# Kernel tuning notes

Measured on AMD Instinct MI355X. Metric: run time of the kernel, lower is better.

## Reference

```python
import jax, jax.numpy as jnp
import numpy as np
import math

MU = 0.1
NU = 10.0
UNITS = [512] * 8
FEATURES = 1024
BATCH = 8192
EPS = 1e-5


def _norm(x):
    return jnp.linalg.norm(x) + EPS


def _cayley(W):
    # Cayley orthogonalization; matches the torch reference (recursive transpose for wide matrices).
    cout, cin = W.shape
    if cin > cout:
        return _cayley(W.T).T
    U, V = W[:cin], W[cin:]
    I = jnp.eye(cin, dtype=W.dtype)
    A = U - U.T + V.T @ V
    iIpA = jnp.linalg.inv(I + A)
    return jnp.concatenate([iIpA @ (I - A), -2.0 * V @ iIpA], axis=0)


def setup_inputs() -> dict:
    key = jax.random.key(0)
    ks = jax.random.split(key, 5)
    sum_units = sum(UNITS)
    # xavier-normal-ish scales
    x = jax.random.normal(ks[0], (BATCH, FEATURES), jnp.float32)
    Fq = jax.random.normal(ks[1], (sum_units, FEATURES), jnp.float32) * math.sqrt(2.0 / (sum_units + FEATURES))
    fq = _norm(Fq).reshape(1)  # init.constant_(fq, norm(Fq))
    by = jnp.zeros((FEATURES,), jnp.float32)
    nz = UNITS[0]
    Fr0 = jax.random.normal(ks[2], (nz, nz), jnp.float32) * math.sqrt(2.0 / (nz + nz))
    Fr_rest = jax.random.normal(ks[3], (len(UNITS) - 1, nz, 2 * nz), jnp.float32) * math.sqrt(2.0 / (nz + 2 * nz))
    fr0 = _norm(Fr0).reshape(1)
    fr_rest = jnp.linalg.norm(Fr_rest, axis=(1, 2)) + EPS
    fr = jnp.concatenate([fr0, fr_rest])
    b = jnp.zeros((len(UNITS), nz), jnp.float32)
    return {"x": x, "Fq": Fq, "fq": fq, "by": by, "Fr0": Fr0, "Fr_rest": Fr_rest, "fr": fr, "b": b}


def reference(x, Fq, fq, by, Fr0, Fr_rest, fr, b):
    sqrt_gam = math.sqrt(NU - MU)
    sqrt2 = math.sqrt(2.0)
    # per-forward Cayley orthogonalization (training path)
    Q = _cayley(fq[0] * Fq / _norm(Fq))  # (sum_units, features)
    Rs = [_cayley(fr[0] * Fr0 / _norm(Fr0))]
    for k in range(Fr_rest.shape[0]):
        Rs.append(_cayley(fr[k + 1] * Fr_rest[k] / _norm(Fr_rest[k])))

    xh = sqrt_gam * (x @ Q.T)  # (B, sum_units)
    yh = []
    hk_1 = xh[..., :0]  # empty start
    idx = 0
    for k, nz in enumerate(UNITS):
        xk = xh[..., idx:idx + nz]
        pre = sqrt2 * (jnp.concatenate([xk, hk_1], axis=-1) @ Rs[k].T) + b[k]
        gh = sqrt2 * (jax.nn.relu(pre) @ Rs[k])  # (B, nz + nz_prev)
        hk = gh[..., :nz] - xk
        gk = gh[..., nz:]
        yh.append(hk_1 - gk)
        idx += nz
        hk_1 = hk
    yh.append(hk_1)
    yh = jnp.concatenate(yh, axis=-1)  # (B, sum_units)
    return 0.5 * ((MU + NU) * x + sqrt_gam * (yh @ Q)) + by
```

## Files before the change

### kernel.cpp

```cpp
#include <hip/hip_runtime.h>
#include <math.h>


using s8v = __attribute__((ext_vector_type(8))) short;
using f4v = __attribute__((ext_vector_type(4))) float;
typedef unsigned short ush;
typedef unsigned int uint32;

#define DEV __device__ __forceinline__

DEV float b2f(ush u){ union{unsigned int i; float f;} v; v.i = ((unsigned int)u)<<16; return v.f; }
DEV ush f2b(float f){
  union{float f; unsigned int i;} v; v.f = f;
  unsigned int u = v.i;
  return (ush)((u + 0x7fffu + ((u>>16)&1u)) >> 16);
}

typedef __attribute__((address_space(1))) void gvoid;
typedef __attribute__((address_space(3))) void lvoid;
DEV void gload16(const void* g, void* l){
  __builtin_amdgcn_global_load_lds((gvoid*)g, (lvoid*)l, 16, 0, 0);
}

DEV void st16(ush* dst, const ush* a){
  *(int4*)dst = *(const int4*)a; *(int4*)(dst+8) = *(const int4*)(a+8);
}

struct GA {
  const ush *A0h, *A0l; long lda0;
  const ush *A1h, *A1l; long lda1; int ksplit;
  const ush *Bh, *Bl; long ldb;
  int K, M, N;
  float alpha, beta;
  long sA, sB, sO, sD;
  void *o0,*o1,*o2,*o3,*o4;
  const void *e0,*e1;
  long ldo0, ldo1, ldE;
};

enum { E_F32=0, E_BF16=1, E_BF16T2=2, E_SPLIT=3, E_QW=4, E_PRE=5, E_GH=6, E_OUT=7 };

template<int BM, int BN, int EPI, bool SPLIT, bool TRX>
__global__ __launch_bounds__(256) void gemm_k(GA gq, GA gr, int zsplit)
{
  constexpr int AH = BM*32;
  constexpr int BH = BN*32;
  constexpr int PANEL = (AH+BH) * (SPLIT ? 2 : 1);
  constexpr int DEPTH = (PANEL <= 6144) ? 2 : 1;
  constexpr int NBUF  = DEPTH + 2;
  constexpr int TBN = TRX ? 64*65*2 : 0;
  constexpr int SMN = (NBUF*PANEL > TBN) ? NBUF*PANEL : TBN;
  __shared__ ush smem[SMN] __attribute__((aligned(16)));
  uint32* tb = (uint32*)smem;

  constexpr int LPS = (BM/64 + BN/64) * (SPLIT ? 2 : 1);

  GA g; int bz;
  if ((int)blockIdx.z < zsplit){ g = gq; bz = blockIdx.z; }
  else                         { g = gr; bz = blockIdx.z - zsplit; }

  const int gx = gridDim.x, gy = gridDim.y;
  const int lin = blockIdx.y*gx + blockIdx.x;
  const int per = gx*8;
  const int grp = lin / per;
  const int rem = lin - grp*per;
  int gh = gy - grp*8; if (gh > 8) gh = 8;
  const int by = grp*8 + rem % gh;
  const int bx = rem / gh;
  const int m0 = by * BM;
  const int n0 = bx * BN;
  if (m0 >= g.M || n0 >= g.N) return;

  const int t = threadIdx.x;
  const int lane = t & 63;
  const int wave = t >> 6;
  const int wm = (wave >> 1) * (BM/2);
  const int wn = (wave & 1) * (BN/2);
  constexpr int MT = BM/32;
  constexpr int NT = BN/32;

  const ush* Ah  = g.A0h + (long)bz*g.sA;
  const ush* Alp = SPLIT ? g.A0l + (long)bz*g.sA : nullptr;
  const ush* Bhp = g.Bh  + (long)bz*g.sB;
  const ush* Blp = SPLIT ? g.Bl  + (long)bz*g.sB : nullptr;

  f4v acc[MT][NT];
  #pragma unroll
  for (int i=0;i<MT;i++)
    #pragma unroll
    for (int j=0;j<NT;j++) acc[i][j] = f4v{0.f,0.f,0.f,0.f};

  const int sr  = lane >> 2;
  const int scg = lane & 3;

  auto STAGE = [&](int k0, int nb){
    ush* dA  = smem + nb*PANEL;
    ush* dB  = dA + AH;
    ush* dAl = dB + BH;
    ush* dBl = dAl + AH;
    #pragma unroll
    for (int p = 0; p < BM/64; ++p) {
      const int lr = wave*16 + sr + p*64;
      const int gc = scg ^ ((lr>>1)&3);
      const int kc = k0 + gc*8;
      long aoff; const ush* gp;
      if (kc < g.ksplit){ aoff = (long)(m0+lr)*g.lda0 + kc;               gp = Ah + aoff; }
      else              { aoff = (long)(m0+lr)*g.lda1 + (kc - g.ksplit);  gp = g.A1h + aoff; }
      gload16(gp, &dA[(wave*16 + p*64)*32]);
      if (SPLIT) gload16(Alp + aoff, &dAl[(wave*16 + p*64)*32]);
    }
    #pragma unroll
    for (int p = 0; p < BN/64; ++p) {
      const int lr = wave*16 + sr + p*64;
      const int gc = scg ^ ((lr>>1)&3);
      const long boff = (long)(n0+lr)*g.ldb + k0 + gc*8;
      gload16(Bhp + boff, &dB[(wave*16 + p*64)*32]);
      if (SPLIT) gload16(Blp + boff, &dBl[(wave*16 + p*64)*32]);
    }
  };

  STAGE(0, 0);
  if (DEPTH == 2 && g.K > 32) STAGE(32, 1);
  int cur = 0;
  for (int k0 = 0; k0 < g.K; k0 += 32) {
    const int rem_steps = ((g.K - k0) >> 5) - 1;
    if (DEPTH == 2) {
      if (rem_steps >= 2) {
        const int nb = (cur+2 >= NBUF) ? cur+2-NBUF : cur+2;
        STAGE(k0 + 64, nb);
        asm volatile("s_waitcnt vmcnt(%0)" :: "n"(2*LPS) : "memory");
      } else if (rem_steps == 1) {
        asm volatile("s_waitcnt vmcnt(%0)" :: "n"(LPS) : "memory");
      } else {
        asm volatile("s_waitcnt vmcnt(0)" ::: "memory");
      }
    } else {
      if (rem_steps >= 1) {
        const int nb = (cur+1 >= NBUF) ? cur+1-NBUF : cur+1;
        STAGE(k0 + 32, nb);
        asm volatile("s_waitcnt vmcnt(%0)" :: "n"(LPS) : "memory");
      } else {
        asm volatile("s_waitcnt vmcnt(0)" ::: "memory");
      }
    }
    __builtin_amdgcn_sched_barrier(0);
    __builtin_amdgcn_s_barrier();
    __builtin_amdgcn_sched_barrier(0);

    const ush* rA  = smem + cur*PANEL;
    const ush* rB  = rA + AH;
    const ush* rAl = rB + BH;
    const ush* rBl = rAl + AH;

    const int fr = lane & 15;
    const int cc = lane >> 4;
    s8v af[MT], bf_[NT];
    #pragma unroll
    for (int i=0;i<MT;i++){ const int row = wm + i*16 + fr;
      af[i] = *(const s8v*)(&rA[row*32 + ((cc ^ ((row>>1)&3))<<3)]); }
    #pragma unroll
    for (int j=0;j<NT;j++){ const int row = wn + j*16 + fr;
      bf_[j] = *(const s8v*)(&rB[row*32 + ((cc ^ ((row>>1)&3))<<3)]); }
    #pragma unroll
    for (int i=0;i<MT;i++)
      #pragma unroll
      for (int j=0;j<NT;j++)
        acc[i][j] = __builtin_amdgcn_mfma_f32_16x16x32_bf16(af[i], bf_[j], acc[i][j], 0,0,0);
    if (SPLIT) {
      s8v al2[MT], bl2[NT];
      #pragma unroll
      for (int j=0;j<NT;j++){ const int row = wn + j*16 + fr;
        bl2[j] = *(const s8v*)(&rBl[row*32 + ((cc ^ ((row>>1)&3))<<3)]); }
      #pragma unroll
      for (int i=0;i<MT;i++){ const int row = wm + i*16 + fr;
        al2[i] = *(const s8v*)(&rAl[row*32 + ((cc ^ ((row>>1)&3))<<3)]); }
      #pragma unroll
      for (int i=0;i<MT;i++)
        #pragma unroll
        for (int j=0;j<NT;j++)
          acc[i][j] = __builtin_amdgcn_mfma_f32_16x16x32_bf16(af[i], bl2[j], acc[i][j], 0,0,0);
      #pragma unroll
      for (int i=0;i<MT;i++)
        #pragma unroll
        for (int j=0;j<NT;j++)
          acc[i][j] = __builtin_amdgcn_mfma_f32_16x16x32_bf16(al2[i], bf_[j], acc[i][j], 0,0,0);
    }
    cur = (cur+1 >= NBUF) ? 0 : cur+1;
  }

  if constexpr (TRX) __syncthreads();

  #pragma unroll
  for (int i=0;i<MT;i++)
    #pragma unroll
    for (int j=0;j<NT;j++)
      #pragma unroll
      for (int r=0;r<4;r++) {
        const int lrow = wm + i*16 + ((lane>>4)<<2) + r;
        const int lcol = wn + j*16 + (lane & 15);
        const int grow = m0 + lrow;
        const int gcol = n0 + lcol;
        float v = g.alpha * acc[i][j][r];
        if constexpr (EPI == E_F32) {
          if (g.e0) v += g.beta * ((const float*)g.e0)[(long)bz*g.sD + (long)grow*g.ldo0 + gcol];
          ((float*)g.o0)[(long)bz*g.sO + (long)grow*g.ldo0 + gcol] = v;
        } else if constexpr (EPI == E_BF16) {
          if (g.e0) v += g.beta * b2f(((const ush*)g.e0)[(long)bz*g.sD + (long)grow*g.ldo0 + gcol]);
          ((ush*)g.o0)[(long)bz*g.sO + (long)grow*g.ldo0 + gcol] = f2b(v);
        } else if constexpr (EPI == E_BF16T2) {
          if (g.e0) v += g.beta * b2f(((const ush*)g.e0)[(long)bz*g.sD + (long)grow*g.ldo0 + gcol]);
          ush hv = f2b(v);
          ((ush*)g.o0)[(long)bz*g.sO + (long)grow*g.ldo0 + gcol] = hv;
          tb[lrow*65 + lcol] = hv;
        } else if constexpr (EPI == E_SPLIT) {
          if (g.e0) v += g.beta * ((const float*)g.e0)[(long)bz*g.sD + (long)grow*g.ldo0 + gcol];
          if (g.o0) ((float*)g.o0)[(long)bz*g.sO + (long)grow*g.ldo0 + gcol] = v;
          ush hv = f2b(v);
          ush lv = f2b(v - b2f(hv));
          ((ush*)g.o1)[(long)bz*g.sO + (long)grow*g.ldo0 + gcol] = hv;
          ((ush*)g.o2)[(long)bz*g.sO + (long)grow*g.ldo0 + gcol] = lv;
          if (TRX) tb[lrow*65 + lcol] = (uint32)hv | ((uint32)lv<<16);
        } else if constexpr (EPI == E_QW) {
          ush hv = f2b(v);
          ((ush*)g.o0)[(long)bz*g.sO + (long)grow*g.ldo0 + gcol] = hv;
          tb[lrow*65 + lcol] = hv;
        } else if constexpr (EPI == E_PRE) {
          v += ((const float*)g.e0)[gcol];
          v = v > 0.f ? v : 0.f;
          ((ush*)g.o0)[(long)grow*g.ldo0 + gcol] = f2b(v);
        } else if constexpr (EPI == E_GH) {
          if (gcol < 512) {
            float h = v - b2f(((const ush*)g.e0)[(long)grow*g.ldE + gcol]);
            ush hb = f2b(h);
            ((ush*)g.o0)[(long)grow*512 + gcol] = hb;
            if (g.o2) ((ush*)g.o2)[(long)grow*4096 + gcol] = hb;
          } else {
            float y = b2f(((const ush*)g.e1)[(long)grow*512 + (gcol-512)]) - v;
            ((ush*)g.o1)[(long)grow*4096 + (gcol-512)] = f2b(y);
          }
        } else if constexpr (EPI == E_OUT) {
          float o = 0.5f*(10.1f*((const float*)g.e0)[(long)grow*1024 + gcol] + v)
                  + ((const float*)g.e1)[gcol];
          ((float*)g.o0)[(long)grow*1024 + gcol] = o;
        }
      }

  if constexpr (TRX) {
    __syncthreads();
    const int tr  = t >> 2;
    const int seg = t & 3;
    uint32 vals[16];
    #pragma unroll
    for (int u=0;u<16;u++) vals[u] = tb[(seg*16+u)*65 + tr];
    ush hb[16] __attribute__((aligned(16)));
    ush lb[16] __attribute__((aligned(16)));
    #pragma unroll
    for (int u=0;u<16;u++){ hb[u] = (ush)(vals[u]&0xffffu); lb[u] = (ush)(vals[u]>>16); }
    const long bT = (long)bz*g.sO + (long)(n0+tr)*g.ldo1 + m0 + seg*16;
    if constexpr (EPI == E_BF16T2) {
      st16((ush*)g.o1 + bT, hb);
    } else if constexpr (EPI == E_SPLIT) {
      if (g.o3) { st16((ush*)g.o3 + bT, hb); st16((ush*)g.o4 + bT, lb); }
    } else if constexpr (EPI == E_QW) {
      st16((ush*)g.o1 + bT, hb);
    }
  }
}


__global__ __launch_bounds__(256) void k_norms(const float* __restrict__ Fq,
    const float* __restrict__ Fr0, const float* __restrict__ Frr, float* s2){
  const int y = blockIdx.y;
  const float* p; long cnt4;
  if (y==0){ p=Fq; cnt4=1048576l; }
  else if (y==1){ p=Fr0; cnt4=65536l; }
  else { p=Frr + (long)(y-2)*524288; cnt4=131072l; }
  float s = 0.f;
  for (long i = (long)blockIdx.x*256 + threadIdx.x; i < cnt4; i += (long)gridDim.x*256){
    float4 v = ((const float4*)p)[i];
    s += v.x*v.x + v.y*v.y + v.z*v.z + v.w*v.w;
  }
  #pragma unroll
  for (int o=32;o>0;o>>=1) s += __shfl_down(s, o, 64);
  __shared__ float red[4];
  if ((threadIdx.x & 63)==0) red[threadIdx.x>>6] = s;
  __syncthreads();
  if (threadIdx.x==0) atomicAdd(&s2[y], red[0]+red[1]+red[2]+red[3]);
}

__global__ void k_scales(const float* s2, const float* fq, const float* fr, float* sc){
  int t = threadIdx.x;
  if (t < 9){
    float v = (t==0)? fq[0] : fr[t-1];
    sc[t] = v / (sqrtf(s2[t]) + 1e-5f);
  }
}

__global__ __launch_bounds__(256) void k_buildT(const float* __restrict__ Fq,
    const float* __restrict__ Frr, const float* sc,
    ush* Vh, ush* Vl, ush* Vth, ush* Vtl,
    ush* Wrh, ush* Wrl, ush* WrTh, ush* WrTl){
  __shared__ uint32 tb[64*65];
  const int z = blockIdx.z;
  const int r = threadIdx.x >> 2;
  const int cs = (threadIdx.x & 3)*16;
  ush hh[16] __attribute__((aligned(16)));
  ush ll[16] __attribute__((aligned(16)));
  if (z==0){
    const long r0 = (long)blockIdx.y*64, c0 = (long)blockIdx.x*64;
    const float s = sc[0];
    const float* src = &Fq[(1024+r0+r)*1024 + c0 + cs];
    #pragma unroll
    for (int u=0;u<16;u++){
      float v = s*src[u];
      ush h = f2b(v); ush l = f2b(v - b2f(h));
      hh[u]=h; ll[u]=l;
      tb[r*65 + cs + u] = (uint32)h | ((uint32)l<<16);
    }
    st16(&Vh[(r0+r)*1024 + c0 + cs], hh);
    st16(&Vl[(r0+r)*1024 + c0 + cs], ll);
    __syncthreads();
    const int tr = threadIdx.x>>2, seg = threadIdx.x&3;
    #pragma unroll
    for (int u=0;u<16;u++){
      uint32 v = tb[(seg*16+u)*65 + tr];
      hh[u]=(ush)(v&0xffffu); ll[u]=(ush)(v>>16);
    }
    st16(&Vth[(c0+tr)*3072 + r0 + seg*16], hh);
    st16(&Vtl[(c0+tr)*3072 + r0 + seg*16], ll);
  } else {
    if (blockIdx.x>=8 || blockIdx.y>=8) return;
    const int k = z-1;
    const long r0 = (long)blockIdx.y*64, c0 = (long)blockIdx.x*64;
    const float s = sc[2+k];
    const float* src = &Frr[(long)k*524288 + (r0+r)*1024 + 512 + c0 + cs];
    #pragma unroll
    for (int u=0;u<16;u++){
      float v = s*src[u];
      ush h = f2b(v); ush l = f2b(v - b2f(h));
      hh[u]=h; ll[u]=l;
      tb[r*65 + cs + u] = (uint32)h | ((uint32)l<<16);
    }
    st16(&Wrh[(long)k*262144 + (r0+r)*512 + c0 + cs], hh);
    st16(&Wrl[(long)k*262144 + (r0+r)*512 + c0 + cs], ll);
    __syncthreads();
    const int tr = threadIdx.x>>2, seg = threadIdx.x&3;
    #pragma unroll
    for (int u=0;u<16;u++){
      uint32 v = tb[(seg*16+u)*65 + tr];
      hh[u]=(ush)(v&0xffffu); ll[u]=(ush)(v>>16);
    }
    st16(&WrTh[(long)k*262144 + (c0+tr)*512 + r0 + seg*16], hh);
    st16(&WrTl[(long)k*262144 + (c0+tr)*512 + r0 + seg*16], ll);
  }
}

__global__ __launch_bounds__(256) void k_asmT(const float* __restrict__ Fq,
    const float* __restrict__ Fr0, const float* __restrict__ Frr,
    const float* sc, const float* __restrict__ PP,
    ush* Mh, ush* Ml, ush* MTh, ush* MTl){
  __shared__ uint32 tb[64*65];
  const int z = blockIdx.z;
  const int r = threadIdx.x >> 2;
  const int cs = (threadIdx.x & 3)*16;
  const long ROFF = 1048576l, RS = 262144l;
  long r0 = (long)blockIdx.y*64, c0 = (long)blockIdx.x*64;
  const float* dsrc; const float* msrc; const float* psrc = nullptr;
  float s; long obase; long old_; float sgn;
  if (z==0){
    s = sc[0]; sgn = 1.f;
    dsrc = &Fq[(r0+r)*1024 + c0 + cs];
    msrc = &Fq[(c0+r)*1024 + r0 + cs];
    psrc = &PP[(r0+r)*1024 + c0 + cs];
    obase = 0; old_ = 1024;
  } else {
    if (blockIdx.x>=8 || blockIdx.y>=8) return;
    const int b = z-1;
    if (b==0){
      s = sc[1]; sgn = 1.f;
      dsrc = &Fr0[(r0+r)*512 + c0 + cs];
      msrc = &Fr0[(c0+r)*512 + r0 + cs];
    } else {
      s = sc[1+b]; sgn = -1.f;
      const float* W = Frr + (long)(b-1)*524288;
      dsrc = &W[(r0+r)*1024 + c0 + cs];
      msrc = &W[(c0+r)*1024 + r0 + cs];
      psrc = &PP[ROFF + (long)(b-1)*RS + (r0+r)*512 + c0 + cs];
    }
    obase = ROFF + (long)b*RS; old_ = 512;
  }
  #pragma unroll
  for (int u=0;u<16;u++) tb[r*65 + cs + u] = __float_as_uint(msrc[u]);
  __syncthreads();
  ush hh[16] __attribute__((aligned(16)));
  ush ll[16] __attribute__((aligned(16)));
  #pragma unroll
  for (int u=0;u<16;u++){
    const int c = cs + u;
    float mir = __uint_as_float(tb[c*65 + r]);
    float a = sgn * s * (dsrc[u] - mir);
    if (psrc) a += psrc[u];
    float m = ((r0 + r == c0 + c) ? 1.f : 0.f) + a;
    ush h = f2b(m); ush l = f2b(m - b2f(h));
    hh[u]=h; ll[u]=l;
  }
  st16(&Mh[obase + (r0+r)*old_ + c0 + cs], hh);
  st16(&Ml[obase + (r0+r)*old_ + c0 + cs], ll);
  __syncthreads();
  #pragma unroll
  for (int u=0;u<16;u++) tb[r*65 + cs + u] = (uint32)hh[u] | ((uint32)ll[u]<<16);
  __syncthreads();
  const int tr = threadIdx.x>>2, seg = threadIdx.x&3;
  #pragma unroll
  for (int u=0;u<16;u++){
    uint32 v = tb[(seg*16+u)*65 + tr];
    hh[u]=(ush)(v&0xffffu); ll[u]=(ush)(v>>16);
  }
  st16(&MTh[obase + (c0+tr)*old_ + r0 + seg*16], hh);
  st16(&MTl[obase + (c0+tr)*old_ + r0 + seg*16], ll);
}

__global__ __launch_bounds__(256) void k_rowabs(const float* __restrict__ T2, float* bmax){
  const int y = blockIdx.y;
  const float* row; int n;
  if (y==0){ row = T2 + (long)blockIdx.x*1024; n = 1024; }
  else { if (blockIdx.x >= 512) return;
         row = T2 + 1048576l + (long)(y-1)*262144 + (long)blockIdx.x*512; n = 512; }
  float s=0.f;
  for (int i=threadIdx.x;i<n;i+=256) s += fabsf(row[i]);
  #pragma unroll
  for (int o=32;o>0;o>>=1) s += __shfl_down(s,o,64);
  __shared__ float red[4];
  if ((threadIdx.x&63)==0) red[threadIdx.x>>6]=s;
  __syncthreads();
  if (threadIdx.x==0){
    float tot = red[0]+red[1]+red[2]+red[3];
    atomicMax((unsigned int*)&bmax[y], __float_as_uint(tot));
  }
}

__global__ void k_makec(const float* bmax, float* cvl){
  int t=threadIdx.x;
  if (t<9){
    float bnd = sqrtf(fmaxf(bmax[t], 1.f));
    cvl[t] = 1.9f/(1.f + bnd);
  }
}

__global__ __launch_bounds__(256) void k_initX(const ush* __restrict__ Mh,
    const ush* __restrict__ MTh, const float* cvl, ush* Xh, ush* XTh){
  long i = (long)blockIdx.x*256 + threadIdx.x;
  int b = (i < 1048576l) ? 0 : 1 + (int)((i - 1048576l) >> 18);
  float c = cvl[b];
  Xh[i]  = f2b(c * b2f(MTh[i]));
  XTh[i] = f2b(c * b2f(Mh[i]));
}

__global__ __launch_bounds__(256) void k_promote(const ush* __restrict__ Xh,
    float* Xf, ush* Xl, ush* XTl){
  long i = (long)blockIdx.x*256 + threadIdx.x;
  Xf[i] = b2f(Xh[i]);
  Xl[i] = 0; XTl[i] = 0;
}

__global__ __launch_bounds__(256) void k_topT(const ush* __restrict__ Xh, const ush* __restrict__ Xl,
    ush* Qb, ush* QTb, ush* RK, ush* RKT){
  __shared__ uint32 tb[64*65];
  const int z = blockIdx.z;
  const int r = threadIdx.x >> 2;
  const int cs = (threadIdx.x & 3)*16;
  const long ROFF = 1048576l, RS = 262144l;
  long r0 = (long)blockIdx.y*64, c0 = (long)blockIdx.x*64;
  ush hh[16] __attribute__((aligned(16)));
  if (z==0){
    const long base = (r0+r)*1024 + c0 + cs;
    #pragma unroll
    for (int u=0;u<16;u++){
      float v = 2.f*(b2f(Xh[base+u]) + b2f(Xl[base+u])) - ((r0+r == c0+cs+u)?1.f:0.f);
      hh[u] = f2b(v);
      tb[r*65 + cs + u] = hh[u];
    }
    st16(&Qb[(r0+r)*1024 + c0 + cs], hh);
    __syncthreads();
    const int tr = threadIdx.x>>2, seg = threadIdx.x&3;
    #pragma unroll
    for (int u=0;u<16;u++) hh[u] = (ush)tb[(seg*16+u)*65 + tr];
    st16(&QTb[(c0+tr)*4096 + r0 + seg*16], hh);
  } else {
    if (blockIdx.x>=8 || blockIdx.y>=8) return;
    const int b = z-1;
    const long base = ROFF + (long)b*RS + (r0+r)*512 + c0 + cs;
    #pragma unroll
    for (int u=0;u<16;u++){
      float v = 2.f*(b2f(Xh[base+u]) + b2f(Xl[base+u])) - ((r0+r == c0+cs+u)?1.f:0.f);
      hh[u] = f2b(v);
      tb[r*65 + cs + u] = hh[u];
    }
    st16(&RKT[(long)b*524288 + (r0+r)*512 + c0 + cs], hh);
    __syncthreads();
    const int tr = threadIdx.x>>2, seg = threadIdx.x&3;
    #pragma unroll
    for (int u=0;u<16;u++) hh[u] = (ush)tb[(seg*16+u)*65 + tr];
    st16(&RK[(long)b*524288 + (c0+tr)*1024 + r0 + seg*16], hh);
  }
}

__global__ __launch_bounds__(256) void k_f2bf(const float* __restrict__ in, ush* __restrict__ o){
  long i = ((long)blockIdx.x*256 + threadIdx.x)*8;
  float4 a = *(const float4*)(in+i);
  float4 b = *(const float4*)(in+i+4);
  ush u[8] __attribute__((aligned(16)));
  u[0]=f2b(a.x);u[1]=f2b(a.y);u[2]=f2b(a.z);u[3]=f2b(a.w);
  u[4]=f2b(b.x);u[5]=f2b(b.y);u[6]=f2b(b.z);u[7]=f2b(b.w);
  *(int4*)(o+i) = *(const int4*)u;
}


static GA mk(const ush* Ah, const ush* Al, long lda,
             const ush* Bh, const ush* Bl, long ldb,
             int K, int M, int N, float alpha){
  GA g{}; g.ksplit=1<<30; g.A0h=Ah; g.A0l=Al; g.lda0=lda;
  g.Bh=Bh; g.Bl=Bl; g.ldb=ldb; g.K=K; g.M=M; g.N=N; g.alpha=alpha; g.beta=0.f;
  return g;
}

extern "C" void kernel_launch(void* const* d_in, const int* in_sizes, int n_in,
                              void* d_out, int out_size, void* d_ws, size_t ws_size,
                              hipStream_t stream)
{
  (void)in_sizes; (void)n_in; (void)out_size; (void)ws_size;
  const float* x   = (const float*)d_in[0];
  const float* Fq  = (const float*)d_in[1];
  const float* fqp = (const float*)d_in[2];
  const float* by  = (const float*)d_in[3];
  const float* Fr0 = (const float*)d_in[4];
  const float* Frr = (const float*)d_in[5];
  const float* frp = (const float*)d_in[6];
  const float* bp  = (const float*)d_in[7];
  float* out = (float*)d_out;

  const float SQG = sqrtf(10.0f - 0.1f);
  const float SQ2 = sqrtf(2.0f);
  const long UN = 3145728l;
  const long ROFF = 1048576l, RS = 262144l;

  char* base = (char*)d_ws;
  size_t off = 0;
  auto alloc = [&](size_t bytes)->char*{
    char* p = base + off; off = (off + bytes + 255) & ~(size_t)255; return p;
  };

  ush* Qb  = (ush*)alloc(4194304l*2);
  ush* QTb = (ush*)alloc(4194304l*2);
  ush* RK  = (ush*)alloc(4194304l*2);
  ush* RKT = (ush*)alloc(4194304l*2);
  ush* xbf = (ush*)alloc(8388608l*2);
  float* scal = (float*)alloc(256*4);
  float* s2   = scal;
  float* bmax = scal + 16;
  float* cvl  = scal + 32;
  float* sc   = scal + 48;

  const size_t scratch0 = off;
  ush* Vh   = (ush*)alloc(UN*2);
  ush* Vl   = (ush*)alloc(UN*2);
  ush* Vth  = (ush*)alloc(UN*2);
  ush* Vtl  = (ush*)alloc(UN*2);
  ush* Wrh  = (ush*)alloc(1835008l*2);
  ush* Wrl  = (ush*)alloc(1835008l*2);
  ush* WrTh = (ush*)alloc(1835008l*2);
  ush* WrTl = (ush*)alloc(1835008l*2);
  float* PPf = (float*)alloc(UN*4);
  ush* Mh  = (ush*)alloc(UN*2);
  ush* Ml  = (ush*)alloc(UN*2);
  ush* MTh = (ush*)alloc(UN*2);
  ush* MTl = (ush*)alloc(UN*2);
  ush* Sh  = (ush*)alloc(UN*2);
  ush* XhA = (ush*)alloc(UN*2);
  ush* XhB = (ush*)alloc(UN*2);
  ush* XlA = (ush*)alloc(UN*2);
  ush* XlB = (ush*)alloc(UN*2);
  ush* XThA = (ush*)alloc(UN*2);
  ush* XThB = (ush*)alloc(UN*2);
  ush* XTlA = (ush*)alloc(UN*2);
  ush* XTlB = (ush*)alloc(UN*2);
  float* XfA = (float*)alloc(UN*4);
  float* XfB = (float*)alloc(UN*4);
  ush* Yh  = (ush*)alloc(UN*2);
  ush* Yl  = (ush*)alloc(UN*2);

  ush* Xh[2]  = {XhA, XhB};
  ush* Xl[2]  = {XlA, XlB};
  ush* XTh[2] = {XThA, XThB};
  ush* XTl[2] = {XTlA, XTlB};
  float* Xf[2] = {XfA, XfB};

  dim3 B256(256);
  GA ga{}, gr{};

  (void)hipMemsetAsync(scal, 0, 1024, stream);
  k_norms<<<dim3(256,9),B256,0,stream>>>(Fq, Fr0, Frr, s2);
  k_scales<<<1,16,0,stream>>>(s2, fqp, frp, sc);

  k_buildT<<<dim3(16,48,8),B256,0,stream>>>(Fq, Frr, sc, Vh,Vl,Vth,Vtl, Wrh,Wrl,WrTh,WrTl);

  ga = mk(Vth,Vtl,3072, Vth,Vtl,3072, 3072,1024,1024, 1.f); ga.o0=PPf; ga.ldo0=1024;
  gr = mk(Wrh,Wrl,512, Wrh,Wrl,512, 512,512,512, 1.f);
  gr.sA=RS; gr.sB=RS; gr.o0=PPf+ROFF; gr.sO=RS; gr.ldo0=512;
  gemm_k<64,64,E_F32,true,false><<<dim3(16,16,8),B256,0,stream>>>(ga,gr,1);

  k_asmT<<<dim3(16,16,9),B256,0,stream>>>(Fq, Fr0, Frr, sc, PPf, Mh,Ml,MTh,MTl);

  ga = mk(Mh,nullptr,1024, Mh,nullptr,1024, 1024,1024,1024, 1.f); ga.o0=Sh; ga.ldo0=1024;
  gr = mk(Mh+ROFF,nullptr,512, Mh+ROFF,nullptr,512, 512,512,512, 1.f);
  gr.sA=RS; gr.sB=RS; gr.o0=Sh+ROFF; gr.sO=RS; gr.ldo0=512;
  gemm_k<64,64,E_BF16,false,false><<<dim3(16,16,9),B256,0,stream>>>(ga,gr,1);

  ga = mk(Sh,nullptr,1024, Sh,nullptr,1024, 1024,1024,1024, 1.f); ga.o0=PPf; ga.ldo0=1024;
  gr = mk(Sh+ROFF,nullptr,512, Sh+ROFF,nullptr,512, 512,512,512, 1.f);
  gr.sA=RS; gr.sB=RS; gr.o0=PPf+ROFF; gr.sO=RS; gr.ldo0=512;
  gemm_k<64,64,E_F32,false,false><<<dim3(16,16,9),B256,0,stream>>>(ga,gr,1);
  k_rowabs<<<dim3(1024,9),B256,0,stream>>>(PPf, bmax);
  k_makec<<<1,16,0,stream>>>(bmax, cvl);
  k_initX<<<12288,B256,0,stream>>>(Mh, MTh, cvl, Xh[0], XTh[0]);

  int cur = 0;
  for (int it=0; it<9; ++it){
    int nxt = cur^1;
    ga = mk(XTh[cur],nullptr,1024, Mh,nullptr,1024, 1024,1024,1024, 1.f); ga.o0=Yh; ga.ldo0=1024;
    gr = mk(XTh[cur]+ROFF,nullptr,512, Mh+ROFF,nullptr,512, 512,512,512, 1.f);
    gr.sA=RS; gr.sB=RS; gr.o0=Yh+ROFF; gr.sO=RS; gr.ldo0=512;
    gemm_k<64,64,E_BF16,false,false><<<dim3(16,16,9),B256,0,stream>>>(ga,gr,1);

    ga = mk(Xh[cur],nullptr,1024, Yh,nullptr,1024, 1024,1024,1024, -1.f);
    ga.beta=2.f; ga.e0=Xh[cur];
    ga.o0=Xh[nxt]; ga.o1=XTh[nxt]; ga.ldo0=1024; ga.ldo1=1024;
    gr = mk(Xh[cur]+ROFF,nullptr,512, Yh+ROFF,nullptr,512, 512,512,512, -1.f);
    gr.beta=2.f; gr.e0=Xh[cur]+ROFF; gr.sD=RS;
    gr.sA=RS; gr.sB=RS; gr.sO=RS;
    gr.o0=Xh[nxt]+ROFF; gr.o1=XTh[nxt]+ROFF; gr.ldo0=512; gr.ldo1=512;
    gemm_k<64,64,E_BF16T2,false,true><<<dim3(16,16,9),B256,0,stream>>>(ga,gr,1);
    cur = nxt;
  }

  k_promote<<<12288,B256,0,stream>>>(Xh[cur], Xf[cur], Xl[cur], XTl[cur]);
  for (int it=0; it<2; ++it){
    int nxt = cur^1;
    ga = mk(XTh[cur],XTl[cur],1024, Mh,Ml,1024, 1024,1024,1024, 1.f);
    ga.o1=Yh; ga.o2=Yl; ga.ldo0=1024;
    gr = mk(XTh[cur]+ROFF,XTl[cur]+ROFF,512, Mh+ROFF,Ml+ROFF,512, 512,512,512, 1.f);
    gr.sA=RS; gr.sB=RS; gr.o1=Yh+ROFF; gr.o2=Yl+ROFF; gr.sO=RS; gr.ldo0=512;
    gemm_k<64,64,E_SPLIT,true,false><<<dim3(16,16,9),B256,0,stream>>>(ga,gr,1);

    ga = mk(Xh[cur],Xl[cur],1024, Yh,Yl,1024, 1024,1024,1024, -1.f);
    ga.beta=2.f; ga.e0=Xf[cur];
    ga.o0=Xf[nxt]; ga.o1=Xh[nxt]; ga.o2=Xl[nxt]; ga.o3=XTh[nxt]; ga.o4=XTl[nxt];
    ga.ldo0=1024; ga.ldo1=1024;
    gr = mk(Xh[cur]+ROFF,Xl[cur]+ROFF,512, Yh+ROFF,Yl+ROFF,512, 512,512,512, -1.f);
    gr.beta=2.f; gr.e0=Xf[cur]+ROFF; gr.sD=RS;
    gr.sA=RS; gr.sB=RS; gr.sO=RS;
    gr.o0=Xf[nxt]+ROFF; gr.o1=Xh[nxt]+ROFF; gr.o2=Xl[nxt]+ROFF;
    gr.o3=XTh[nxt]+ROFF; gr.o4=XTl[nxt]+ROFF;
    gr.ldo0=512; gr.ldo1=512;
    gemm_k<64,64,E_SPLIT,true,true><<<dim3(16,16,9),B256,0,stream>>>(ga,gr,1);
    cur = nxt;
  }

  k_topT<<<dim3(16,16,9),B256,0,stream>>>(Xh[cur], Xl[cur], Qb, QTb, RK, RKT);

  ga = mk(Vh,Vl,1024, XTh[cur],XTl[cur],1024, 1024,3072,1024, -2.f);
  ga.o0=Qb + 1048576l; ga.ldo0=1024; ga.o1=QTb + 1024; ga.ldo1=4096;
  gr = mk(WrTh,WrTl,512, XTh[cur]+ROFF+RS, XTl[cur]+ROFF+RS, 512, 512,512,512, -2.f);
  gr.sA=RS; gr.sB=RS; gr.sO=524288;
  gr.o0=RKT + 524288 + 262144; gr.ldo0=512;
  gr.o1=RK + 524288 + 512; gr.ldo1=1024;
  gemm_k<64,64,E_QW,true,true><<<dim3(16,48,8),B256,0,stream>>>(ga,gr,1);

  off = scratch0;
  ush* xh  = (ush*)alloc(33554432l*2);
  ush* yh  = (ush*)alloc(33554432l*2);
  ush* pre = (ush*)alloc(4194304l*2);
  ush* h0  = (ush*)alloc(4194304l*2);
  ush* h1  = (ush*)alloc(4194304l*2);

  k_f2bf<<<4096,B256,0,stream>>>(x, xbf);
  ga = mk(xbf,nullptr,1024, Qb,nullptr,1024, 1024,8192,4096, SQG);
  ga.o0=xh; ga.ldo0=4096;
  gemm_k<128,128,E_BF16,false,false><<<dim3(32,64,1),B256,0,stream>>>(ga,ga,1);

  for (int k=0;k<8;++k){
    ush* hprev = (k==0)? nullptr : (((k-1)&1) ? h1 : h0);
    ush* hnew  = (k&1) ? h1 : h0;
    GA gp_ = mk(xh + (long)k*512, nullptr, 4096,
                (k==0)? RKT : RK + (long)k*524288, nullptr, (k==0)?512:1024,
                (k==0)?512:1024, 8192, 512, SQ2);
    gp_.ksplit = 512; gp_.A1h = hprev; gp_.lda1 = 512;
    gp_.e0 = bp + (long)k*512; gp_.o0 = pre; gp_.ldo0 = 512;
    gemm_k<128,64,E_PRE,false,false><<<dim3(8,64,1),B256,0,stream>>>(gp_,gp_,1);

    GA gg = mk(pre, nullptr, 512,
               (k==0)? RK : RKT + (long)k*524288, nullptr, (k==0)?1024:512,
               512, 8192, (k==0)?512:1024, SQ2);
    gg.e0 = xh + (long)k*512; gg.ldE = 4096;
    gg.e1 = hprev;
    gg.o0 = hnew;
    gg.o1 = (k>=1)? (void*)(yh + (long)(k-1)*512) : nullptr;
    gg.o2 = (k==7)? (void*)(yh + 3584) : nullptr;
    if (k==0) gemm_k<128,64,E_GH,false,false><<<dim3(8,64,1),B256,0,stream>>>(gg,gg,1);
    else      gemm_k<128,128,E_GH,false,false><<<dim3(8,64,1),B256,0,stream>>>(gg,gg,1);
  }

  ga = mk(yh,nullptr,4096, QTb,nullptr,4096, 4096,8192,1024, SQG);
  ga.e0=x; ga.e1=by; ga.o0=out; ga.ldo0=1024;
  gemm_k<128,128,E_OUT,false,false><<<dim3(8,64,1),B256,0,stream>>>(ga,ga,1);
}
```

Before: 1.464 ms.

## Fuse Newton-Schulz iterations into one persistent kernel with grid barriers

Replaces the 18 separate GEMM launches of the nine bf16 Newton-Schulz iterations with a single persistent kernel of 768 blocks. The blocks sync through a hierarchical atomic grid barrier in global memory (32-block groups, then a global counter). This removes per-launch overhead and tail effects. It relies on all 768 blocks being co-resident, otherwise it deadlocks. It also lowers the shared-memory double-buffer threshold in the generic GEMM template.

New measurement: 3.192 ms. 2.18x slower.

```diff
diff --git a/kernel.cpp b/kernel.cpp
--- a/kernel.cpp
+++ b/kernel.cpp
@@ -46,7 +46,7 @@
   constexpr int AH = BM*32;
   constexpr int BH = BN*32;
   constexpr int PANEL = (AH+BH) * (SPLIT ? 2 : 1);
-  constexpr int DEPTH = (PANEL <= 6144) ? 2 : 1;
+  constexpr int DEPTH = (PANEL <= 4096) ? 2 : 1;
   constexpr int NBUF  = DEPTH + 2;
   constexpr int TBN = TRX ? 64*65*2 : 0;
   constexpr int SMN = (NBUF*PANEL > TBN) ? NBUF*PANEL : TBN;
@@ -267,6 +267,147 @@
   }
 }
 
+__global__ __launch_bounds__(256) void ns_fused(
+    const ush* __restrict__ Mh, ush* XhA, ush* XThA, ush* XhB, ush* XThB,
+    ush* Yh, uint32* bar, int iters)
+{
+  constexpr int PANEL = 4096;
+  constexpr int NBUF  = 4;
+  __shared__ ush smem[NBUF*PANEL] __attribute__((aligned(16)));
+  uint32* tb = (uint32*)smem;
+
+  const int b = blockIdx.x;
+  const int tri = b/3, rph = b - tri*3;
+  int m0, n0, ld, K; long base;
+  if (rph == 0){
+    m0 = (tri>>4)<<6; n0 = (tri&15)<<6; base = 0; ld = 1024; K = 1024;
+  } else {
+    const int rj = tri*2 + rph - 1;
+    const int z = rj>>6, idx = rj&63;
+    m0 = (idx>>3)<<6; n0 = (idx&7)<<6;
+    base = 1048576l + (long)z*262144l; ld = 512; K = 512;
+  }
+
+  const int t = threadIdx.x, lane = t&63, wave = t>>6;
+  const int wm = (wave>>1)*32, wn = (wave&1)*32;
+  const int sr = lane>>2, scg = lane&3;
+  const int fr = lane&15, cc = lane>>4;
+
+  int barno = 0;
+  auto gbar = [&](){
+    __syncthreads();
+    if (t == 0){
+      const int grp = b >> 5;
+      uint32 v = __hip_atomic_fetch_add(&bar[64 + grp*32], 1u,
+                    __ATOMIC_RELEASE, __HIP_MEMORY_SCOPE_AGENT);
+      if (v == 31u){
+        __hip_atomic_store(&bar[64 + grp*32], 0u,
+                    __ATOMIC_RELAXED, __HIP_MEMORY_SCOPE_AGENT);
+        uint32 r = __hip_atomic_fetch_add(&bar[16], 1u,
+                    __ATOMIC_ACQ_REL, __HIP_MEMORY_SCOPE_AGENT);
+        if (r == 23u){
+          __hip_atomic_store(&bar[16], 0u,
+                    __ATOMIC_RELAXED, __HIP_MEMORY_SCOPE_AGENT);
+          __hip_atomic_fetch_add(&bar[32], 1u,
+                    __ATOMIC_RELEASE, __HIP_MEMORY_SCOPE_AGENT);
+        }
+      }
+      while ((int)__hip_atomic_load(&bar[32],
+                    __ATOMIC_ACQUIRE, __HIP_MEMORY_SCOPE_AGENT) <= barno)
+        __builtin_amdgcn_s_sleep(2);
+      __threadfence();
+    }
+    __syncthreads();
+    ++barno;
+  };
+
+  auto run_gemm = [&](const ush* A, const ush* B, bool g2,
+                      const ush* e0, ush* o0, ush* oT){
+    f4v acc[2][2];
+    #pragma unroll
+    for (int i=0;i<2;i++)
+      #pragma unroll
+      for (int j=0;j<2;j++) acc[i][j] = f4v{0.f,0.f,0.f,0.f};
+    auto STAGE = [&](int k0, int nb){
+      ush* dA = smem + nb*PANEL;
+      ush* dB = dA + 2048;
+      const int lr = wave*16 + sr;
+      const int gc = scg ^ ((lr>>1)&3);
+      gload16(A + (long)(m0+lr)*ld + k0 + gc*8, &dA[lr*32]);
+      gload16(B + (long)(n0+lr)*ld + k0 + gc*8, &dB[lr*32]);
+    };
+    STAGE(0,0); STAGE(32,1);
+    int cur = 0;
+    for (int k0 = 0; k0 < K; k0 += 32){
+      const int rem = ((K - k0) >> 5) - 1;
+      if (rem >= 2){ STAGE(k0+64, (cur+2)&3);
+        asm volatile("s_waitcnt vmcnt(4)" ::: "memory"); }
+      else if (rem == 1){ asm volatile("s_waitcnt vmcnt(2)" ::: "memory"); }
+      else { asm volatile("s_waitcnt vmcnt(0)" ::: "memory"); }
+      __builtin_amdgcn_sched_barrier(0);
+      __builtin_amdgcn_s_barrier();
+      __builtin_amdgcn_sched_barrier(0);
+      const ush* rA = smem + cur*PANEL;
+      const ush* rB = rA + 2048;
+      s8v af[2], bf_[2];
+      #pragma unroll
+      for (int i=0;i<2;i++){ const int row = wm+i*16+fr;
+        af[i] = *(const s8v*)&rA[row*32 + ((cc ^ ((row>>1)&3))<<3)]; }
+      #pragma unroll
+      for (int j=0;j<2;j++){ const int row = wn+j*16+fr;
+        bf_[j] = *(const s8v*)&rB[row*32 + ((cc ^ ((row>>1)&3))<<3)]; }
+      #pragma unroll
+      for (int i=0;i<2;i++)
+        #pragma unroll
+        for (int j=0;j<2;j++)
+          acc[i][j] = __builtin_amdgcn_mfma_f32_16x16x32_bf16(af[i],bf_[j],acc[i][j],0,0,0);
+      cur = (cur+1)&3;
+    }
+    if (g2) __syncthreads();
+    #pragma unroll
+    for (int i=0;i<2;i++)
+      #pragma unroll
+      for (int j=0;j<2;j++)
+        #pragma unroll
+        for (int r=0;r<4;r++){
+          const int lrow = wm + i*16 + ((lane>>4)<<2) + r;
+          const int lcol = wn + j*16 + fr;
+          const long off = (long)(m0+lrow)*ld + n0 + lcol;
+          if (!g2){
+            o0[off] = f2b(acc[i][j][r]);
+          } else {
+            float v = 2.f*b2f(e0[off]) - acc[i][j][r];
+            ush hv = f2b(v);
+            o0[off] = hv;
+            tb[lrow*65 + lcol] = hv;
+          }
+        }
+    if (g2){
+      __syncthreads();
+      const int tr = t>>2, seg = t&3;
+      uint32 vals[16];
+      #pragma unroll
+      for (int u=0;u<16;u++) vals[u] = tb[(seg*16+u)*65 + tr];
+      ush hb[16] __attribute__((aligned(16)));
+      #pragma unroll
+      for (int u=0;u<16;u++) hb[u] = (ush)vals[u];
+      st16(oT + (long)(n0+tr)*ld + m0 + seg*16, hb);
+    }
+  };
+
+  ush* X[2]  = {XhA, XhB};
+  ush* XT[2] = {XThA, XThB};
+  int cur = 0;
+  for (int it = 0; it < iters; ++it){
+    run_gemm(XT[cur] + base, Mh + base, false, nullptr, Yh + base, nullptr);
+    gbar();
+    run_gemm(X[cur] + base, Yh + base, true, X[cur] + base,
+             X[cur^1] + base, XT[cur^1] + base);
+    if (it != iters-1) gbar();
+    cur ^= 1;
+  }
+}
+
 
 __global__ __launch_bounds__(256) void k_norms(const float* __restrict__ Fq,
     const float* __restrict__ Fr0, const float* __restrict__ Frr, float* s2){
@@ -560,6 +701,7 @@
   float* bmax = scal + 16;
   float* cvl  = scal + 32;
   float* sc   = scal + 48;
+  uint32* bar = (uint32*)alloc(4096);
 
   const size_t scratch0 = off;
   ush* Vh   = (ush*)alloc(UN*2);
@@ -599,6 +741,7 @@
   GA ga{}, gr{};
 
   (void)hipMemsetAsync(scal, 0, 1024, stream);
+  (void)hipMemsetAsync(bar, 0, 4096, stream);
   k_norms<<<dim3(256,9),B256,0,stream>>>(Fq, Fr0, Frr, s2);
   k_scales<<<1,16,0,stream>>>(s2, fqp, frp, sc);
 
@@ -624,24 +767,8 @@
   k_makec<<<1,16,0,stream>>>(bmax, cvl);
   k_initX<<<12288,B256,0,stream>>>(Mh, MTh, cvl, Xh[0], XTh[0]);
 
-  int cur = 0;
-  for (int it=0; it<9; ++it){
-    int nxt = cur^1;
-    ga = mk(XTh[cur],nullptr,1024, Mh,nullptr,1024, 1024,1024,1024, 1.f); ga.o0=Yh; ga.ldo0=1024;
-    gr = mk(XTh[cur]+ROFF,nullptr,512, Mh+ROFF,nullptr,512, 512,512,512, 1.f);
-    gr.sA=RS; gr.sB=RS; gr.o0=Yh+ROFF; gr.sO=RS; gr.ldo0=512;
-    gemm_k<64,64,E_BF16,false,false><<<dim3(16,16,9),B256,0,stream>>>(ga,gr,1);
-
-    ga = mk(Xh[cur],nullptr,1024, Yh,nullptr,1024, 1024,1024,1024, -1.f);
-    ga.beta=2.f; ga.e0=Xh[cur];
-    ga.o0=Xh[nxt]; ga.o1=XTh[nxt]; ga.ldo0=1024; ga.ldo1=1024;
-    gr = mk(Xh[cur]+ROFF,nullptr,512, Yh+ROFF,nullptr,512, 512,512,512, -1.f);
-    gr.beta=2.f; gr.e0=Xh[cur]+ROFF; gr.sD=RS;
-    gr.sA=RS; gr.sB=RS; gr.sO=RS;
-    gr.o0=Xh[nxt]+ROFF; gr.o1=XTh[nxt]+ROFF; gr.ldo0=512; gr.ldo1=512;
-    gemm_k<64,64,E_BF16T2,false,true><<<dim3(16,16,9),B256,0,stream>>>(ga,gr,1);
-    cur = nxt;
-  }
+  ns_fused<<<768,B256,0,stream>>>(Mh, XhA, XThA, XhB, XThB, Yh, bar, 9);
+  int cur = 1;
 
   k_promote<<<12288,B256,0,stream>>>(Xh[cur], Xf[cur], Xl[cur], XTl[cur]);
   for (int it=0; it<2; ++it){
```
